# Optimization experiments

Hardware: AMD Instinct MI355X
Metric: run time of the kernel (lower is better)

Reference implementation:

```python
import jax, jax.numpy as jnp
import numpy as np


def setup_inputs() -> dict:
    key = jax.random.key(0)
    ks = jax.random.split(key, 8)
    B, N, E, D, C = 64, 1024, 16384, 1024, 128
    x = jax.random.normal(ks[0], (B, D), dtype=jnp.float32)
    edge_index = jax.random.randint(ks[1], (2, E), 0, N, dtype=jnp.int64)
    W_emb = jax.random.normal(ks[2], (D, C), dtype=jnp.float32) * (2.0 / D) ** 0.5
    b_emb = jnp.zeros((C,), dtype=jnp.float32)
    W_conv = jax.random.normal(ks[3], (C, C), dtype=jnp.float32) * (2.0 / C) ** 0.5
    b_conv = jnp.zeros((C,), dtype=jnp.float32)
    W_cls = jax.random.normal(ks[4], (C, 1), dtype=jnp.float32) * (2.0 / C) ** 0.5
    b_cls = jnp.zeros((1,), dtype=jnp.float32)
    return {"x": x, "edge_index": edge_index, "W_emb": W_emb, "b_emb": b_emb,
            "W_conv": W_conv, "b_conv": b_conv, "W_cls": W_cls, "b_cls": b_cls,
            "n_nodes": N, "n_conv": 4}


def reference(x, edge_index, W_emb, b_emb, W_conv, b_conv, W_cls, b_cls, n_nodes, n_conv):
    B = x.shape[0]
    total = B * n_nodes
    # tile each flattened sample across all nodes of its graph copy  [B*N, D]
    x_batch = jnp.repeat(x.reshape(B, -1), n_nodes, axis=0)
    # batched edge index: disjoint union of B copies of the graph  [2, B*E]
    offs = (jnp.arange(B, dtype=edge_index.dtype) * n_nodes)[None, :, None]
    ei = (edge_index[:, None, :] + offs).reshape(2, -1)
    src, dst = ei[0], ei[1]
    # embedding: Linear + ReLU
    h = jax.nn.relu(x_batch @ W_emb + b_emb)
    # n_conv applications of the SAME GCNConv (no self loops, no normalization) + ReLU
    def conv(h, _):
        hw = h @ W_conv                                   # [B*N, C]
        agg = jax.ops.segment_sum(hw[src], dst, num_segments=total)
        return jax.nn.relu(agg + b_conv), None
    h, _ = jax.lax.scan(conv, h, None, length=n_conv)
    # node 0 of each graph copy, then classifier
    out = h[::n_nodes] @ W_cls + b_cls                    # [B, 1]
    return out
```

## Files before the change

kernel.cpp:

```cpp
#include <hip/hip_runtime.h>
#include <cstdint>
#include <cstddef>

constexpr int Bn = 64;
constexpr int Nn = 1024;
constexpr int Dn = 1024;
constexpr int Cn = 128;
constexpr int En = 16384;
constexpr int DMAX = 64;
constexpr int NB3 = 192;

typedef short s16x8 __attribute__((ext_vector_type(8)));
typedef float f32x4 __attribute__((ext_vector_type(4)));

__device__ __forceinline__ uint32_t f2bf(float f) {
    uint32_t u = __float_as_uint(f);
    return (u + 0x7fffu + ((u >> 16) & 1u)) >> 16;
}

__global__ __launch_bounds__(256) void k_prep(const float* __restrict__ x,
                                              const float* __restrict__ We,
                                              const float* __restrict__ Wc,
                                              const int* __restrict__ ei32,
                                              float* __restrict__ pws,
                                              unsigned short* __restrict__ Wt,
                                              unsigned int* __restrict__ epk,
                                              int* __restrict__ hists,
                                              int* __restrict__ f3,
                                              int* __restrict__ Mm,
                                              int* __restrict__ n3cur,
                                              int* __restrict__ meta) {
    int bid = blockIdx.x, tid = threadIdx.x;
    if (bid < 256) {
        __shared__ float sx[256];
        __shared__ float sp[256];
        int b = bid >> 2, q = bid & 3;
        int c = tid & 127, h2 = tid >> 7;
        sx[tid] = x[b * Dn + q * 256 + tid];
        __syncthreads();
        float acc = 0.f;
        int d0 = q * 256 + h2 * 128;
        int dl = h2 * 128;
#pragma unroll 8
        for (int i = 0; i < 128; ++i) acc += sx[dl + i] * We[(d0 + i) * Cn + c];
        sp[h2 * 128 + c] = acc;
        __syncthreads();
        if (h2 == 0) pws[(b * 4 + q) * Cn + c] = sp[c] + sp[128 + c];
    } else if (bid < 320) {
        int i = (bid - 256) * 256 + tid;
        int n = i >> 7, k = i & 127;
        Wt[i] = (unsigned short)f2bf(Wc[k * Cn + n]);
    } else if (bid < 336) {
        int hb = bid - 320;
        __shared__ int hloc[Nn];
        __shared__ int det;
#pragma unroll
        for (int r = 0; r < 4; ++r) hloc[r * 256 + tid] = 0;
        if (tid == 0) det = 0;
        __syncthreads();
        int base = hb * 1024;
        int hw = 0;
#pragma unroll
        for (int r = 0; r < 4; ++r) { int i = base + r * 256 + tid; hw |= ei32[2 * i + 1]; }
        if (hw) atomicOr(&det, 1);
        __syncthreads();
        bool i64 = (det == 0);
#pragma unroll
        for (int r = 0; r < 4; ++r) {
            int i = base + r * 256 + tid;
            int s, d;
            if (i64) {
                s = ((const int2*)ei32)[i].x & (Nn - 1);
                d = ((const int2*)ei32)[En + i].x & (Nn - 1);
            } else {
                s = ei32[i] & (Nn - 1);
                d = ei32[En + i] & (Nn - 1);
            }
            epk[i] = (unsigned)s | ((unsigned)d << 16);
            atomicAdd(&hloc[d], 1);
            if (d == 0) f3[s] = 1;
        }
        __syncthreads();
#pragma unroll
        for (int r = 0; r < 4; ++r) hists[hb * Nn + r * 256 + tid] = hloc[r * 256 + tid];
    } else if (bid < 340) {
        int4 z = {0, 0, 0, 0};
        int4* M4 = (int4*)Mm;
#pragma unroll
        for (int r = 0; r < 16; ++r) M4[(bid - 336) * 4096 + r * 256 + tid] = z;
    } else {
        int4 z = {0, 0, 0, 0};
        ((int4*)n3cur)[tid] = z;
        if (tid == 0) meta[4] = 0;
    }
}

__global__ __launch_bounds__(1024) void k_build(const int* __restrict__ hists,
                                                const unsigned int* __restrict__ epk,
                                                const int* __restrict__ f3,
                                                int* __restrict__ f2,
                                                int* __restrict__ Mm,
                                                int* __restrict__ n3cur,
                                                int* __restrict__ n3src,
                                                int* __restrict__ e0,
                                                int* __restrict__ L3,
                                                int* __restrict__ meta,
                                                const float* __restrict__ pws,
                                                const float* __restrict__ be,
                                                const float* __restrict__ Wc,
                                                float* __restrict__ g) {
    int bid = blockIdx.x, t = threadIdx.x;
    if (bid < 16) {
        __shared__ int sInd[Nn];
        int v = 0;
#pragma unroll
        for (int h = 0; h < 16; ++h) v += hists[h * Nn + t];
        sInd[t] = v;
        __syncthreads();
        unsigned e = epk[bid * 1024 + t];
        int s = e & 0xffff, d = e >> 16;
        int dd = sInd[s]; if (dd > DMAX - 1) dd = DMAX - 1;
        atomicAdd(&Mm[d * DMAX + dd], 1);
        if (f3[d] == 1) {
            f2[s] = 1;
            int p = atomicAdd(&n3cur[d], 1);
            if (p < NB3) n3src[d * NB3 + p] = s;
        }
        if (d == 0) {
            int p = atomicAdd(&meta[4], 1);
            if (p < 1024) e0[p] = s;
        }
    } else if (bid == 16) {
        __shared__ int c3;
        if (t == 0) c3 = 0;
        __syncthreads();
        if (f3[t] == 1) { int p = atomicAdd(&c3, 1); L3[p] = t; }
        __syncthreads();
        if (t == 0) meta[2] = c3;
    } else {
        __shared__ float se[8][Cn];
        int blk = bid - 17, bi = t >> 7, c = t & 127, b = blk * 8 + bi;
        float e4 = pws[(b * 4 + 0) * Cn + c] + pws[(b * 4 + 1) * Cn + c] +
                   pws[(b * 4 + 2) * Cn + c] + pws[(b * 4 + 3) * Cn + c] + be[c];
        se[bi][c] = fmaxf(e4, 0.f);
        __syncthreads();
        float acc = 0.f;
#pragma unroll 8
        for (int k = 0; k < Cn; ++k) acc += se[bi][k] * Wc[k * Cn + c];
        g[b * Cn + c] = acc;
    }
}

constexpr int PAD = 136;
constexpr int PADR = 72;

__global__ __launch_bounds__(256, 4) void k_conv2M(const float* __restrict__ g,
                                                   float* __restrict__ h2,
                                                   const unsigned short* __restrict__ Wt,
                                                   const float* __restrict__ bc,
                                                   const int* __restrict__ Mm,
                                                   const int* __restrict__ f2) {
    int bidx = blockIdx.x;
    int tile0 = bidx >> 6, b = bidx & 63;
    __shared__ int sL2[Nn];
    __shared__ int sWs[4];
    __shared__ unsigned short sRt[128 * PADR];
    __shared__ unsigned short sMb[32 * PADR];
    __shared__ unsigned short sSb[32 * PAD];
    __shared__ int snode[32];
    int tid = threadIdx.x, lane = tid & 63, w = tid >> 6;
    int m = lane & 15, quad = lane >> 4;

    int n0 = tid * 4;
    int fl0 = (f2[n0] == 1), fl1 = (f2[n0 + 1] == 1), fl2 = (f2[n0 + 2] == 1), fl3 = (f2[n0 + 3] == 1);
    int c = fl0 + fl1 + fl2 + fl3;
    int inc = c;
    for (int off = 1; off < 64; off <<= 1) {
        int nv = __shfl_up(inc, off);
        if (lane >= off) inc += nv;
    }
    if (lane == 63) sWs[w] = inc;
    __syncthreads();
    int wbase = 0;
#pragma unroll
    for (int q = 0; q < 4; ++q) wbase += (q < w) ? sWs[q] : 0;
    int cnt2 = sWs[0] + sWs[1] + sWs[2] + sWs[3];
    int pos = wbase + inc - c;
    if (fl0) sL2[pos++] = n0;
    if (fl1) sL2[pos++] = n0 + 1;
    if (fl2) sL2[pos++] = n0 + 2;
    if (fl3) sL2[pos++] = n0 + 3;

    {
        int cc = tid & 127, dh = tid >> 7;
        float gc = g[b * Cn + cc], bcc = bc[cc];
#pragma unroll
        for (int d = dh * 32; d < dh * 32 + 32; ++d) {
            float r = fmaxf(fmaf((float)d, gc, bcc), 0.f);
            sRt[cc * PADR + d] = (unsigned short)f2bf(r);
        }
    }

    s16x8 bf0[4], bf1[4];
#pragma unroll
    for (int ks = 0; ks < 4; ++ks) {
        int ko = ks * 32 + quad * 8;
        bf0[ks] = *(const s16x8*)&Wt[(w * 32 + m) * Cn + ko];
        bf1[ks] = *(const s16x8*)&Wt[(w * 32 + 16 + m) * Cn + ko];
    }
    __syncthreads();

    for (int tile = tile0; tile * 32 < cnt2; tile += 8) {
        __syncthreads();
        if (tid < 32) {
            int ti = tile * 32 + tid;
            snode[tid] = (ti < cnt2) ? sL2[ti] : -1;
        }
        __syncthreads();
        {
            int row = tid >> 3, seg = tid & 7;
            int node = snode[row];
            unsigned short pk[8];
            if (node >= 0) {
                const int4* mp = (const int4*)&Mm[node * DMAX + seg * 8];
                int4 a = mp[0], bq = mp[1];
                pk[0] = (unsigned short)f2bf((float)a.x);
                pk[1] = (unsigned short)f2bf((float)a.y);
                pk[2] = (unsigned short)f2bf((float)a.z);
                pk[3] = (unsigned short)f2bf((float)a.w);
                pk[4] = (unsigned short)f2bf((float)bq.x);
                pk[5] = (unsigned short)f2bf((float)bq.y);
                pk[6] = (unsigned short)f2bf((float)bq.z);
                pk[7] = (unsigned short)f2bf((float)bq.w);
            } else {
#pragma unroll
                for (int i = 0; i < 8; ++i) pk[i] = 0;
            }
            *(uint4*)&sMb[row * PADR + seg * 8] = *(uint4*)pk;
        }
        __syncthreads();

        f32x4 acc1[2][2];
#pragma unroll
        for (int rt = 0; rt < 2; ++rt)
#pragma unroll
            for (int ct = 0; ct < 2; ++ct) acc1[rt][ct] = (f32x4){0.f, 0.f, 0.f, 0.f};
#pragma unroll
        for (int ks = 0; ks < 2; ++ks) {
            int ko = ks * 32 + quad * 8;
            s16x8 a0 = *(const s16x8*)&sMb[m * PADR + ko];
            s16x8 a1 = *(const s16x8*)&sMb[(16 + m) * PADR + ko];
            s16x8 r0 = *(const s16x8*)&sRt[(w * 32 + m) * PADR + ko];
            s16x8 r1 = *(const s16x8*)&sRt[(w * 32 + 16 + m) * PADR + ko];
            acc1[0][0] = __builtin_amdgcn_mfma_f32_16x16x32_bf16(a0, r0, acc1[0][0], 0, 0, 0);
            acc1[0][1] = __builtin_amdgcn_mfma_f32_16x16x32_bf16(a0, r1, acc1[0][1], 0, 0, 0);
            acc1[1][0] = __builtin_amdgcn_mfma_f32_16x16x32_bf16(a1, r0, acc1[1][0], 0, 0, 0);
            acc1[1][1] = __builtin_amdgcn_mfma_f32_16x16x32_bf16(a1, r1, acc1[1][1], 0, 0, 0);
        }
#pragma unroll
        for (int rt = 0; rt < 2; ++rt)
#pragma unroll
            for (int ct = 0; ct < 2; ++ct) {
                int col = w * 32 + ct * 16 + m;
#pragma unroll
                for (int reg = 0; reg < 4; ++reg) {
                    int row = rt * 16 + quad * 4 + reg;
                    sSb[row * PAD + col] = (unsigned short)f2bf(acc1[rt][ct][reg]);
                }
            }
        __syncthreads();

        f32x4 acc[2][2];
#pragma unroll
        for (int rt = 0; rt < 2; ++rt)
#pragma unroll
            for (int ct = 0; ct < 2; ++ct) acc[rt][ct] = (f32x4){0.f, 0.f, 0.f, 0.f};
#pragma unroll
        for (int ks = 0; ks < 4; ++ks) {
            int ko = ks * 32 + quad * 8;
            s16x8 a0 = *(const s16x8*)&sSb[(0 * 16 + m) * PAD + ko];
            s16x8 a1 = *(const s16x8*)&sSb[(1 * 16 + m) * PAD + ko];
            acc[0][0] = __builtin_amdgcn_mfma_f32_16x16x32_bf16(a0, bf0[ks], acc[0][0], 0, 0, 0);
            acc[0][1] = __builtin_amdgcn_mfma_f32_16x16x32_bf16(a0, bf1[ks], acc[0][1], 0, 0, 0);
            acc[1][0] = __builtin_amdgcn_mfma_f32_16x16x32_bf16(a1, bf0[ks], acc[1][0], 0, 0, 0);
            acc[1][1] = __builtin_amdgcn_mfma_f32_16x16x32_bf16(a1, bf1[ks], acc[1][1], 0, 0, 0);
        }

#pragma unroll
        for (int rt = 0; rt < 2; ++rt)
#pragma unroll
            for (int ct = 0; ct < 2; ++ct) {
                int col = w * 32 + ct * 16 + m;
                float bias = bc[col];
#pragma unroll
                for (int reg = 0; reg < 4; ++reg) {
                    int row = rt * 16 + quad * 4 + reg;
                    int node = snode[row];
                    if (node >= 0)
                        h2[((size_t)b * Nn + node) * Cn + col] = fmaxf(acc[rt][ct][reg] + bias, 0.f);
                }
            }
    }
}

__global__ __launch_bounds__(256) void k_conv34(const float* __restrict__ h2,
                                                const unsigned short* __restrict__ Wt,
                                                const float* __restrict__ bc,
                                                const int* __restrict__ L3,
                                                const int* __restrict__ meta,
                                                const int* __restrict__ n3cur,
                                                const int* __restrict__ n3src,
                                                const int* __restrict__ e0,
                                                const float* __restrict__ Wc,
                                                const float* __restrict__ Wcls,
                                                const float* __restrict__ bcls,
                                                float* __restrict__ out) {
    __shared__ unsigned short sSb[32 * PAD];
    __shared__ int sIdx[32][64];
    __shared__ float sH3[32][Cn];
    __shared__ short smap[Nn];
    __shared__ int snode[32], scnt[32];
    __shared__ float sAgg[8][Cn];
    __shared__ float sred[256];
    __shared__ int sI[256];
    int b = blockIdx.x, tid = threadIdx.x;
    int cnt3 = meta[2];
    int m0 = meta[4]; if (m0 > 1024) m0 = 1024;
    int lim = m0 < 256 ? m0 : 256;
    if (tid < lim) sI[tid] = e0[tid];

    int w = tid >> 6, lane = tid & 63, m = lane & 15, quad = lane >> 4;
    s16x8 bf0[4], bf1[4];
#pragma unroll
    for (int ks = 0; ks < 4; ++ks) {
        int ko = ks * 32 + quad * 8;
        bf0[ks] = *(const s16x8*)&Wt[(w * 32 + m) * Cn + ko];
        bf1[ks] = *(const s16x8*)&Wt[(w * 32 + 16 + m) * Cn + ko];
    }
    int c4 = tid & 31, u = tid >> 5;
    const float4* hb4 = (const float4*)(h2 + (size_t)b * (Nn * Cn));
    float4 aAgg = {0.f, 0.f, 0.f, 0.f};

    for (int tile = 0; tile * 32 < cnt3; ++tile) {
        __syncthreads();
#pragma unroll
        for (int r = 0; r < 4; ++r) smap[tid + 256 * r] = -1;
        if (tid < 32) {
            int ti = tile * 32 + tid;
            int node = (ti < cnt3) ? L3[ti] : -1;
            snode[tid] = node;
            int cnt = (node >= 0) ? n3cur[node] : 0;
            if (cnt > NB3) cnt = NB3;
            scnt[tid] = cnt;
        }
        __syncthreads();
        if (tid < 32 && snode[tid] >= 0) smap[snode[tid]] = (short)tid;
#pragma unroll
        for (int r = 0; r < 8; ++r) {
            int row = w * 8 + r;
            int cnt = scnt[row];
            if (lane < cnt && lane < 64) sIdx[row][lane] = n3src[snode[row] * NB3 + lane];
        }
        __syncthreads();

#pragma unroll
        for (int t0 = 0; t0 < 4; ++t0) {
            int row = u * 4 + t0;
            int cnt = scnt[row];
            float4 a = {0.f, 0.f, 0.f, 0.f};
            int jm = cnt < 64 ? cnt : 64;
            for (int j = 0; j < jm; ++j) {
                float4 v = hb4[sIdx[row][j] * 32 + c4];
                a.x += v.x; a.y += v.y; a.z += v.z; a.w += v.w;
            }
            for (int j = 64; j < cnt; ++j) {
                float4 v = hb4[n3src[snode[row] * NB3 + j] * 32 + c4];
                a.x += v.x; a.y += v.y; a.z += v.z; a.w += v.w;
            }
            uint2 pk;
            pk.x = f2bf(a.x) | (f2bf(a.y) << 16);
            pk.y = f2bf(a.z) | (f2bf(a.w) << 16);
            *(uint2*)&sSb[row * PAD + c4 * 4] = pk;
        }
        __syncthreads();

        f32x4 acc[2][2];
#pragma unroll
        for (int rt = 0; rt < 2; ++rt)
#pragma unroll
            for (int ct = 0; ct < 2; ++ct) acc[rt][ct] = (f32x4){0.f, 0.f, 0.f, 0.f};
#pragma unroll
        for (int ks = 0; ks < 4; ++ks) {
            int ko = ks * 32 + quad * 8;
            s16x8 a0 = *(const s16x8*)&sSb[(0 * 16 + m) * PAD + ko];
            s16x8 a1 = *(const s16x8*)&sSb[(1 * 16 + m) * PAD + ko];
            acc[0][0] = __builtin_amdgcn_mfma_f32_16x16x32_bf16(a0, bf0[ks], acc[0][0], 0, 0, 0);
            acc[0][1] = __builtin_amdgcn_mfma_f32_16x16x32_bf16(a0, bf1[ks], acc[0][1], 0, 0, 0);
            acc[1][0] = __builtin_amdgcn_mfma_f32_16x16x32_bf16(a1, bf0[ks], acc[1][0], 0, 0, 0);
            acc[1][1] = __builtin_amdgcn_mfma_f32_16x16x32_bf16(a1, bf1[ks], acc[1][1], 0, 0, 0);
        }

#pragma unroll
        for (int rt = 0; rt < 2; ++rt)
#pragma unroll
            for (int ct = 0; ct < 2; ++ct) {
                int col = w * 32 + ct * 16 + m;
                float bias = bc[col];
#pragma unroll
                for (int reg = 0; reg < 4; ++reg) {
                    int row = rt * 16 + quad * 4 + reg;
                    sH3[row][col] = fmaxf(acc[rt][ct][reg] + bias, 0.f);
                }
            }
        __syncthreads();

        for (int j = u; j < lim; j += 8) {
            int r2 = smap[sI[j]];
            if (r2 >= 0) {
                float4 v = *(const float4*)&sH3[r2][c4 * 4];
                aAgg.x += v.x; aAgg.y += v.y; aAgg.z += v.z; aAgg.w += v.w;
            }
        }
        for (int j = 256 + u; j < m0; j += 8) {
            int r2 = smap[e0[j]];
            if (r2 >= 0) {
                float4 v = *(const float4*)&sH3[r2][c4 * 4];
                aAgg.x += v.x; aAgg.y += v.y; aAgg.z += v.z; aAgg.w += v.w;
            }
        }
    }

    *(float4*)&sAgg[u][c4 * 4] = aAgg;
    __syncthreads();
    int c = tid & 127, half = tid >> 7;
    if (tid < 128) {
        float s = sAgg[0][c];
#pragma unroll
        for (int q2 = 1; q2 < 8; ++q2) s += sAgg[q2][c];
        sAgg[0][c] = s;
    }
    __syncthreads();
    float s = 0.f;
    int k0 = half * 64;
#pragma unroll 8
    for (int k = k0; k < k0 + 64; ++k) s += sAgg[0][k] * Wc[k * Cn + c];
    sred[tid] = s;
    __syncthreads();
    if (tid < 128) {
        float val = fmaxf(sred[c] + sred[128 + c] + bc[c], 0.f);
        sred[tid] = val * Wcls[c];
    }
    __syncthreads();
    for (int st = 64; st > 0; st >>= 1) {
        if (tid < st) sred[tid] += sred[tid + st];
        __syncthreads();
    }
    if (tid == 0) out[b] = sred[0] + bcls[0];
}

extern "C" void kernel_launch(void* const* d_in, const int* in_sizes, int n_in,
                              void* d_out, int out_size, void* d_ws, size_t ws_size,
                              hipStream_t stream) {
    const float* x    = (const float*)d_in[0];
    const int*   ei32 = (const int*)d_in[1];
    const float* We   = (const float*)d_in[2];
    const float* be   = (const float*)d_in[3];
    const float* Wc   = (const float*)d_in[4];
    const float* bc   = (const float*)d_in[5];
    const float* Wcls = (const float*)d_in[6];
    const float* bcls = (const float*)d_in[7];
    float* out = (float*)d_out;

    char* ws = (char*)d_ws;
    float*          g      = (float*)(ws + 0);
    int*            meta   = (int*)(ws + 32768);
    int*            e0     = (int*)(ws + 36864);
    int*            n3cur  = (int*)(ws + 40960);
    unsigned short* Wt     = (unsigned short*)(ws + 45056);
    float*          pws    = (float*)(ws + 77824);
    int*            f3     = (int*)(ws + 208896);
    int*            f2     = (int*)(ws + 212992);
    unsigned int*   epk    = (unsigned int*)(ws + 217088);
    int*            hists  = (int*)(ws + 282624);
    int*            Mm     = (int*)(ws + 348160);
    int*            n3src  = (int*)(ws + 610304);
    int*            L3     = (int*)(ws + 1396736);
    float*          h2full = (float*)(ws + 1400832);

    k_prep<<<341, 256, 0, stream>>>(x, We, Wc, ei32, pws, Wt, epk, hists, f3, Mm, n3cur, meta);
    k_build<<<25, 1024, 0, stream>>>(hists, epk, f3, f2, Mm, n3cur, n3src, e0, L3, meta,
                                     pws, be, Wc, g);
    k_conv2M<<<8 * Bn, 256, 0, stream>>>(g, h2full, Wt, bc, Mm, f2);
    k_conv34<<<Bn, 256, 0, stream>>>(h2full, Wt, bc, L3, meta, n3cur, n3src, e0,
                                     Wc, Wcls, bcls, out);
}
```

Before: 111.2 us.

## Eliminate k_build kernel by recomputing graph structures per block in shared memory

Removes the k_build launch and its global atomics and buffers (Mm, n3src, L3, e0, f2, g). Each conv block now rebuilds the f2 flags, in-degree, per-tile degree histograms, source lists and node-0 edge list in LDS by scanning all edges, and computes g = relu(emb)·Wc inline. The embedding split is also widened to 8 K-chunks per batch element. This saves one launch and its dependency but makes every block rescan all 16K edges, possibly several times per tile, and raises LDS use (launch bounds drop to 2 blocks per SM).

```diff
diff --git a/kernel.cpp b/kernel.cpp
--- a/kernel.cpp
+++ b/kernel.cpp
@@ -8,7 +8,6 @@
 constexpr int Cn = 128;
 constexpr int En = 16384;
 constexpr int DMAX = 64;
-constexpr int NB3 = 192;
 
 typedef short s16x8 __attribute__((ext_vector_type(8)));
 typedef float f32x4 __attribute__((ext_vector_type(4)));
@@ -26,32 +25,29 @@
                                               unsigned short* __restrict__ Wt,
                                               unsigned int* __restrict__ epk,
                                               int* __restrict__ hists,
-                                              int* __restrict__ f3,
-                                              int* __restrict__ Mm,
-                                              int* __restrict__ n3cur,
-                                              int* __restrict__ meta) {
+                                              int* __restrict__ f3) {
     int bid = blockIdx.x, tid = threadIdx.x;
-    if (bid < 256) {
-        __shared__ float sx[256];
+    if (bid < 512) {
+        __shared__ float sx[128];
         __shared__ float sp[256];
-        int b = bid >> 2, q = bid & 3;
-        int c = tid & 127, h2 = tid >> 7;
-        sx[tid] = x[b * Dn + q * 256 + tid];
+        int b = bid >> 3, q = bid & 7;
+        int c = tid & 127, h = tid >> 7;
+        if (tid < 128) sx[tid] = x[b * Dn + q * 128 + tid];
         __syncthreads();
         float acc = 0.f;
-        int d0 = q * 256 + h2 * 128;
-        int dl = h2 * 128;
+        int kl = h * 64;
+        int d0 = q * 128 + kl;
 #pragma unroll 8
-        for (int i = 0; i < 128; ++i) acc += sx[dl + i] * We[(d0 + i) * Cn + c];
-        sp[h2 * 128 + c] = acc;
-        __syncthreads();
-        if (h2 == 0) pws[(b * 4 + q) * Cn + c] = sp[c] + sp[128 + c];
-    } else if (bid < 320) {
-        int i = (bid - 256) * 256 + tid;
+        for (int i = 0; i < 64; ++i) acc += sx[kl + i] * We[(d0 + i) * Cn + c];
+        sp[h * 128 + c] = acc;
+        __syncthreads();
+        if (h == 0) pws[(b * 8 + q) * Cn + c] = sp[c] + sp[128 + c];
+    } else if (bid < 576) {
+        int i = (bid - 512) * 256 + tid;
         int n = i >> 7, k = i & 127;
         Wt[i] = (unsigned short)f2bf(Wc[k * Cn + n]);
-    } else if (bid < 336) {
-        int hb = bid - 320;
+    } else {
+        int hb = bid - 576;
         __shared__ int hloc[Nn];
         __shared__ int det;
 #pragma unroll
@@ -83,98 +79,61 @@
         __syncthreads();
 #pragma unroll
         for (int r = 0; r < 4; ++r) hists[hb * Nn + r * 256 + tid] = hloc[r * 256 + tid];
-    } else if (bid < 340) {
-        int4 z = {0, 0, 0, 0};
-        int4* M4 = (int4*)Mm;
-#pragma unroll
-        for (int r = 0; r < 16; ++r) M4[(bid - 336) * 4096 + r * 256 + tid] = z;
-    } else {
-        int4 z = {0, 0, 0, 0};
-        ((int4*)n3cur)[tid] = z;
-        if (tid == 0) meta[4] = 0;
-    }
-}
-
-__global__ __launch_bounds__(1024) void k_build(const int* __restrict__ hists,
-                                                const unsigned int* __restrict__ epk,
-                                                const int* __restrict__ f3,
-                                                int* __restrict__ f2,
-                                                int* __restrict__ Mm,
-                                                int* __restrict__ n3cur,
-                                                int* __restrict__ n3src,
-                                                int* __restrict__ e0,
-                                                int* __restrict__ L3,
-                                                int* __restrict__ meta,
-                                                const float* __restrict__ pws,
-                                                const float* __restrict__ be,
-                                                const float* __restrict__ Wc,
-                                                float* __restrict__ g) {
-    int bid = blockIdx.x, t = threadIdx.x;
-    if (bid < 16) {
-        __shared__ int sInd[Nn];
-        int v = 0;
-#pragma unroll
-        for (int h = 0; h < 16; ++h) v += hists[h * Nn + t];
-        sInd[t] = v;
-        __syncthreads();
-        unsigned e = epk[bid * 1024 + t];
-        int s = e & 0xffff, d = e >> 16;
-        int dd = sInd[s]; if (dd > DMAX - 1) dd = DMAX - 1;
-        atomicAdd(&Mm[d * DMAX + dd], 1);
-        if (f3[d] == 1) {
-            f2[s] = 1;
-            int p = atomicAdd(&n3cur[d], 1);
-            if (p < NB3) n3src[d * NB3 + p] = s;
-        }
-        if (d == 0) {
-            int p = atomicAdd(&meta[4], 1);
-            if (p < 1024) e0[p] = s;
-        }
-    } else if (bid == 16) {
-        __shared__ int c3;
-        if (t == 0) c3 = 0;
-        __syncthreads();
-        if (f3[t] == 1) { int p = atomicAdd(&c3, 1); L3[p] = t; }
-        __syncthreads();
-        if (t == 0) meta[2] = c3;
-    } else {
-        __shared__ float se[8][Cn];
-        int blk = bid - 17, bi = t >> 7, c = t & 127, b = blk * 8 + bi;
-        float e4 = pws[(b * 4 + 0) * Cn + c] + pws[(b * 4 + 1) * Cn + c] +
-                   pws[(b * 4 + 2) * Cn + c] + pws[(b * 4 + 3) * Cn + c] + be[c];
-        se[bi][c] = fmaxf(e4, 0.f);
-        __syncthreads();
-        float acc = 0.f;
-#pragma unroll 8
-        for (int k = 0; k < Cn; ++k) acc += se[bi][k] * Wc[k * Cn + c];
-        g[b * Cn + c] = acc;
     }
 }
 
 constexpr int PAD = 136;
 constexpr int PADR = 72;
 
-__global__ __launch_bounds__(256, 4) void k_conv2M(const float* __restrict__ g,
-                                                   float* __restrict__ h2,
+__global__ __launch_bounds__(256, 2) void k_conv2M(const float* __restrict__ pws,
+                                                   const float* __restrict__ be,
+                                                   const float* __restrict__ Wc,
+                                                   const float* __restrict__ bc,
                                                    const unsigned short* __restrict__ Wt,
-                                                   const float* __restrict__ bc,
-                                                   const int* __restrict__ Mm,
-                                                   const int* __restrict__ f2) {
+                                                   const int* __restrict__ f3,
+                                                   const unsigned int* __restrict__ epk,
+                                                   const int* __restrict__ hists,
+                                                   float* __restrict__ h2) {
     int bidx = blockIdx.x;
     int tile0 = bidx >> 6, b = bidx & 63;
+    __shared__ int sInd[Nn];
+    __shared__ unsigned char sF3[Nn];
+    __shared__ unsigned char sF2[Nn];
     __shared__ int sL2[Nn];
     __shared__ int sWs[4];
+    __shared__ float sE[Cn];
+    __shared__ float sGp[256];
+    __shared__ float sG[Cn];
     __shared__ unsigned short sRt[128 * PADR];
     __shared__ unsigned short sMb[32 * PADR];
     __shared__ unsigned short sSb[32 * PAD];
+    __shared__ short smap[Nn];
+    __shared__ int sM[32 * 64];
     __shared__ int snode[32];
     int tid = threadIdx.x, lane = tid & 63, w = tid >> 6;
     int m = lane & 15, quad = lane >> 4;
 
+#pragma unroll 4
+    for (int i = tid; i < Nn; i += 256) {
+        sF3[i] = (f3[i] == 1);
+        sF2[i] = 0;
+        int v = 0;
+#pragma unroll
+        for (int hh = 0; hh < 16; ++hh) v += hists[hh * Nn + i];
+        sInd[i] = v;
+    }
+    __syncthreads();
+#pragma unroll 4
+    for (int i = tid; i < En; i += 256) {
+        unsigned e = epk[i];
+        if (sF3[e >> 16]) sF2[e & 0xffff] = 1;
+    }
+    __syncthreads();
+
     int n0 = tid * 4;
-    int fl0 = (f2[n0] == 1), fl1 = (f2[n0 + 1] == 1), fl2 = (f2[n0 + 2] == 1), fl3 = (f2[n0 + 3] == 1);
-    int c = fl0 + fl1 + fl2 + fl3;
-    int inc = c;
+    int fl0 = sF2[n0], fl1 = sF2[n0 + 1], fl2 = sF2[n0 + 2], fl3 = sF2[n0 + 3];
+    int cflags = fl0 + fl1 + fl2 + fl3;
+    int inc = cflags;
     for (int off = 1; off < 64; off <<= 1) {
         int nv = __shfl_up(inc, off);
         if (lane >= off) inc += nv;
@@ -185,17 +144,35 @@
 #pragma unroll
     for (int q = 0; q < 4; ++q) wbase += (q < w) ? sWs[q] : 0;
     int cnt2 = sWs[0] + sWs[1] + sWs[2] + sWs[3];
-    int pos = wbase + inc - c;
+    int pos = wbase + inc - cflags;
     if (fl0) sL2[pos++] = n0;
     if (fl1) sL2[pos++] = n0 + 1;
     if (fl2) sL2[pos++] = n0 + 2;
     if (fl3) sL2[pos++] = n0 + 3;
 
+    int cc = tid & 127, half = tid >> 7;
+    if (half == 0) {
+        float e4 = be[cc];
+#pragma unroll
+        for (int q = 0; q < 8; ++q) e4 += pws[(b * 8 + q) * Cn + cc];
+        sE[cc] = fmaxf(e4, 0.f);
+    }
+    __syncthreads();
     {
-        int cc = tid & 127, dh = tid >> 7;
-        float gc = g[b * Cn + cc], bcc = bc[cc];
-#pragma unroll
-        for (int d = dh * 32; d < dh * 32 + 32; ++d) {
+        float gp = 0.f;
+        int k0 = half * 64;
+#pragma unroll 8
+        for (int k = k0; k < k0 + 64; ++k) gp += sE[k] * Wc[k * Cn + cc];
+        sGp[half * 128 + cc] = gp;
+    }
+    __syncthreads();
+    if (half == 0) sG[cc] = sGp[cc] + sGp[128 + cc];
+    __syncthreads();
+
+    {
+        float gc = sG[cc], bcc = bc[cc];
+#pragma unroll
+        for (int d = half * 32; d < half * 32 + 32; ++d) {
             float r = fmaxf(fmaf((float)d, gc, bcc), 0.f);
             sRt[cc * PADR + d] = (unsigned short)f2bf(r);
         }
@@ -212,30 +189,33 @@
 
     for (int tile = tile0; tile * 32 < cnt2; tile += 8) {
         __syncthreads();
+#pragma unroll 4
+        for (int i = tid; i < Nn; i += 256) smap[i] = -1;
+#pragma unroll 8
+        for (int i = tid; i < 2048; i += 256) sM[i] = 0;
         if (tid < 32) {
             int ti = tile * 32 + tid;
             snode[tid] = (ti < cnt2) ? sL2[ti] : -1;
         }
         __syncthreads();
+        if (tid < 32 && snode[tid] >= 0) smap[snode[tid]] = (short)tid;
+        __syncthreads();
+#pragma unroll 4
+        for (int i = tid; i < En; i += 256) {
+            unsigned e = epk[i];
+            int r = smap[e >> 16];
+            if (r >= 0) {
+                int s = e & 0xffff;
+                int dd = sInd[s]; if (dd > DMAX - 1) dd = DMAX - 1;
+                atomicAdd(&sM[r * DMAX + dd], 1);
+            }
+        }
+        __syncthreads();
         {
             int row = tid >> 3, seg = tid & 7;
-            int node = snode[row];
             unsigned short pk[8];
-            if (node >= 0) {
-                const int4* mp = (const int4*)&Mm[node * DMAX + seg * 8];
-                int4 a = mp[0], bq = mp[1];
-                pk[0] = (unsigned short)f2bf((float)a.x);
-                pk[1] = (unsigned short)f2bf((float)a.y);
-                pk[2] = (unsigned short)f2bf((float)a.z);
-                pk[3] = (unsigned short)f2bf((float)a.w);
-                pk[4] = (unsigned short)f2bf((float)bq.x);
-                pk[5] = (unsigned short)f2bf((float)bq.y);
-                pk[6] = (unsigned short)f2bf((float)bq.z);
-                pk[7] = (unsigned short)f2bf((float)bq.w);
-            } else {
-#pragma unroll
-                for (int i = 0; i < 8; ++i) pk[i] = 0;
-            }
+#pragma unroll
+            for (int i = 0; i < 8; ++i) pk[i] = (unsigned short)f2bf((float)sM[row * DMAX + seg * 8 + i]);
             *(uint4*)&sMb[row * PADR + seg * 8] = *(uint4*)pk;
         }
         __syncthreads();
@@ -306,30 +286,62 @@
 __global__ __launch_bounds__(256) void k_conv34(const float* __restrict__ h2,
                                                 const unsigned short* __restrict__ Wt,
                                                 const float* __restrict__ bc,
-                                                const int* __restrict__ L3,
-                                                const int* __restrict__ meta,
-                                                const int* __restrict__ n3cur,
-                                                const int* __restrict__ n3src,
-                                                const int* __restrict__ e0,
+                                                const int* __restrict__ f3,
+                                                const unsigned int* __restrict__ epk,
                                                 const float* __restrict__ Wc,
                                                 const float* __restrict__ Wcls,
                                                 const float* __restrict__ bcls,
                                                 float* __restrict__ out) {
+    __shared__ unsigned char sF3[Nn];
+    __shared__ int sL3[Nn];
+    __shared__ int sWs[4];
+    __shared__ int sE0[1024];
+    __shared__ int se0c;
     __shared__ unsigned short sSb[32 * PAD];
-    __shared__ int sIdx[32][64];
+    __shared__ int sIdx[32][96];
+    __shared__ int scnt[32];
     __shared__ float sH3[32][Cn];
     __shared__ short smap[Nn];
-    __shared__ int snode[32], scnt[32];
+    __shared__ int snode[32];
     __shared__ float sAgg[8][Cn];
     __shared__ float sred[256];
-    __shared__ int sI[256];
     int b = blockIdx.x, tid = threadIdx.x;
-    int cnt3 = meta[2];
-    int m0 = meta[4]; if (m0 > 1024) m0 = 1024;
-    int lim = m0 < 256 ? m0 : 256;
-    if (tid < lim) sI[tid] = e0[tid];
-
-    int w = tid >> 6, lane = tid & 63, m = lane & 15, quad = lane >> 4;
+    int lane = tid & 63, w = tid >> 6;
+    int m = lane & 15, quad = lane >> 4;
+
+#pragma unroll 4
+    for (int i = tid; i < Nn; i += 256) sF3[i] = (f3[i] == 1);
+    if (tid == 0) se0c = 0;
+    __syncthreads();
+    int n0 = tid * 4;
+    int fl0 = sF3[n0], fl1 = sF3[n0 + 1], fl2 = sF3[n0 + 2], fl3 = sF3[n0 + 3];
+    int cflags = fl0 + fl1 + fl2 + fl3;
+    int inc = cflags;
+    for (int off = 1; off < 64; off <<= 1) {
+        int nv = __shfl_up(inc, off);
+        if (lane >= off) inc += nv;
+    }
+    if (lane == 63) sWs[w] = inc;
+#pragma unroll 4
+    for (int i = tid; i < En; i += 256) {
+        unsigned e = epk[i];
+        if ((e >> 16) == 0) {
+            int p = atomicAdd(&se0c, 1);
+            if (p < 1024) sE0[p] = e & 0xffff;
+        }
+    }
+    __syncthreads();
+    int wbase = 0;
+#pragma unroll
+    for (int q = 0; q < 4; ++q) wbase += (q < w) ? sWs[q] : 0;
+    int cnt3 = sWs[0] + sWs[1] + sWs[2] + sWs[3];
+    int pos = wbase + inc - cflags;
+    if (fl0) sL3[pos++] = n0;
+    if (fl1) sL3[pos++] = n0 + 1;
+    if (fl2) sL3[pos++] = n0 + 2;
+    if (fl3) sL3[pos++] = n0 + 3;
+    int m0 = se0c; if (m0 > 1024) m0 = 1024;
+
     s16x8 bf0[4], bf1[4];
 #pragma unroll
     for (int ks = 0; ks < 4; ++ks) {
@@ -343,38 +355,34 @@
 
     for (int tile = 0; tile * 32 < cnt3; ++tile) {
         __syncthreads();
-#pragma unroll
-        for (int r = 0; r < 4; ++r) smap[tid + 256 * r] = -1;
+#pragma unroll 4
+        for (int i = tid; i < Nn; i += 256) smap[i] = -1;
         if (tid < 32) {
             int ti = tile * 32 + tid;
-            int node = (ti < cnt3) ? L3[ti] : -1;
-            snode[tid] = node;
-            int cnt = (node >= 0) ? n3cur[node] : 0;
-            if (cnt > NB3) cnt = NB3;
-            scnt[tid] = cnt;
+            snode[tid] = (ti < cnt3) ? sL3[ti] : -1;
+            scnt[tid] = 0;
         }
         __syncthreads();
         if (tid < 32 && snode[tid] >= 0) smap[snode[tid]] = (short)tid;
-#pragma unroll
-        for (int r = 0; r < 8; ++r) {
-            int row = w * 8 + r;
-            int cnt = scnt[row];
-            if (lane < cnt && lane < 64) sIdx[row][lane] = n3src[snode[row] * NB3 + lane];
+        __syncthreads();
+#pragma unroll 4
+        for (int i = tid; i < En; i += 256) {
+            unsigned e = epk[i];
+            int r = smap[e >> 16];
+            if (r >= 0) {
+                int p = atomicAdd(&scnt[r], 1);
+                if (p < 96) sIdx[r][p] = e & 0xffff;
+            }
         }
         __syncthreads();
 
 #pragma unroll
         for (int t0 = 0; t0 < 4; ++t0) {
             int row = u * 4 + t0;
-            int cnt = scnt[row];
+            int cnt = scnt[row]; if (cnt > 96) cnt = 96;
             float4 a = {0.f, 0.f, 0.f, 0.f};
-            int jm = cnt < 64 ? cnt : 64;
-            for (int j = 0; j < jm; ++j) {
+            for (int j = 0; j < cnt; ++j) {
                 float4 v = hb4[sIdx[row][j] * 32 + c4];
-                a.x += v.x; a.y += v.y; a.z += v.z; a.w += v.w;
-            }
-            for (int j = 64; j < cnt; ++j) {
-                float4 v = hb4[n3src[snode[row] * NB3 + j] * 32 + c4];
                 a.x += v.x; a.y += v.y; a.z += v.z; a.w += v.w;
             }
             uint2 pk;
@@ -414,15 +422,8 @@
             }
         __syncthreads();
 
-        for (int j = u; j < lim; j += 8) {
-            int r2 = smap[sI[j]];
-            if (r2 >= 0) {
-                float4 v = *(const float4*)&sH3[r2][c4 * 4];
-                aAgg.x += v.x; aAgg.y += v.y; aAgg.z += v.z; aAgg.w += v.w;
-            }
-        }
-        for (int j = 256 + u; j < m0; j += 8) {
-            int r2 = smap[e0[j]];
+        for (int j = u; j < m0; j += 8) {
+            int r2 = smap[sE0[j]];
             if (r2 >= 0) {
                 float4 v = *(const float4*)&sH3[r2][c4 * 4];
                 aAgg.x += v.x; aAgg.y += v.y; aAgg.z += v.z; aAgg.w += v.w;
@@ -472,25 +473,14 @@
     float* out = (float*)d_out;
 
     char* ws = (char*)d_ws;
-    float*          g      = (float*)(ws + 0);
-    int*            meta   = (int*)(ws + 32768);
-    int*            e0     = (int*)(ws + 36864);
-    int*            n3cur  = (int*)(ws + 40960);
-    unsigned short* Wt     = (unsigned short*)(ws + 45056);
-    float*          pws    = (float*)(ws + 77824);
-    int*            f3     = (int*)(ws + 208896);
-    int*            f2     = (int*)(ws + 212992);
-    unsigned int*   epk    = (unsigned int*)(ws + 217088);
-    int*            hists  = (int*)(ws + 282624);
-    int*            Mm     = (int*)(ws + 348160);
-    int*            n3src  = (int*)(ws + 610304);
-    int*            L3     = (int*)(ws + 1396736);
-    float*          h2full = (float*)(ws + 1400832);
-
-    k_prep<<<341, 256, 0, stream>>>(x, We, Wc, ei32, pws, Wt, epk, hists, f3, Mm, n3cur, meta);
-    k_build<<<25, 1024, 0, stream>>>(hists, epk, f3, f2, Mm, n3cur, n3src, e0, L3, meta,
-                                     pws, be, Wc, g);
-    k_conv2M<<<8 * Bn, 256, 0, stream>>>(g, h2full, Wt, bc, Mm, f2);
-    k_conv34<<<Bn, 256, 0, stream>>>(h2full, Wt, bc, L3, meta, n3cur, n3src, e0,
-                                     Wc, Wcls, bcls, out);
+    unsigned short* Wt     = (unsigned short*)(ws + 0);
+    int*            f3     = (int*)(ws + 32768);
+    unsigned int*   epk    = (unsigned int*)(ws + 36864);
+    int*            hists  = (int*)(ws + 102400);
+    float*          pws    = (float*)(ws + 167936);
+    float*          h2full = (float*)(ws + 430080);
+
+    k_prep<<<592, 256, 0, stream>>>(x, We, Wc, ei32, pws, Wt, epk, hists, f3);
+    k_conv2M<<<8 * Bn, 256, 0, stream>>>(pws, be, Wc, bc, Wt, f3, epk, hists, h2full);
+    k_conv34<<<Bn, 256, 0, stream>>>(h2full, Wt, bc, f3, epk, Wc, Wcls, bcls, out);
 }
```

New measurement: 156.5 us. 1.41x slower.
